# Optimization experiments

Measured on AMD Instinct MI355X. Metric: run time of the kernel, lower is better.

## Reference

```python
import jax, jax.numpy as jnp
import numpy as np
import math

NUM_HEADS = 8
DROPOUT_RATE = 0.1
D_IN = 32
D_PROJ = 32 * 16  # 512
B, SQ, SK = 8, 2048, 2048


def setup_inputs() -> dict:
    key = jax.random.key(0)
    ks = jax.random.split(key, 10)
    inv = 1.0 / math.sqrt(D_IN)
    return {
        "query": jax.random.normal(ks[0], (B, SQ, D_IN), dtype=jnp.float32),
        "key": jax.random.normal(ks[1], (B, SK, D_IN), dtype=jnp.float32),
        "value": jax.random.normal(ks[2], (B, SK, D_IN), dtype=jnp.float32),
        "mask": jax.random.randint(ks[3], (B, 1, 1, SK), 0, 2, dtype=jnp.int32),
        "Wq": jax.random.normal(ks[4], (D_PROJ, D_IN), dtype=jnp.float32) * inv,
        "bq": jax.random.normal(ks[5], (D_PROJ,), dtype=jnp.float32) * 0.02,
        "Wk": jax.random.normal(ks[6], (D_PROJ, D_IN), dtype=jnp.float32) * inv,
        "bk": jax.random.normal(ks[7], (D_PROJ,), dtype=jnp.float32) * 0.02,
        "Wv": jax.random.normal(ks[8], (D_PROJ, D_IN), dtype=jnp.float32) * inv,
        "bv": jax.random.normal(ks[9], (D_PROJ,), dtype=jnp.float32) * 0.02,
    }


def _split_heads(x):
    # [B, S, H*D] -> [B, H, S, D]
    b, s, _ = x.shape
    return x.reshape(b, s, NUM_HEADS, D_PROJ // NUM_HEADS).transpose(0, 2, 1, 3)


def reference(query, key, value, mask, Wq, bq, Wk, bk, Wv, bv):
    q = _split_heads(query @ Wq.T + bq)   # [B, H, Sq, D]
    k = _split_heads(key @ Wk.T + bk)     # [B, H, Sk, D]
    v = _split_heads(value @ Wv.T + bv)   # [B, H, Sk, D]

    head_dim = q.shape[-1]
    # mask only feeds this scalar; max(1-p, (1-p)/(Sm2*Sm3)) == 1-p for Sm2*Sm3 >= 1
    keep = 1.0 - DROPOUT_RATE
    scale_factor = jnp.maximum(jnp.float32(keep),
                               jnp.float32(keep / (mask.shape[2] * mask.shape[3])))

    scores = jnp.einsum("bhqd,bhkd->bhqk", q, k) * (scale_factor / math.sqrt(head_dim))
    probs = jax.nn.softmax(scores, axis=-1)
    # dropout treated as identity (eval mode) for a deterministic reference
    out = jnp.einsum("bhqk,bhkd->bhqd", probs, v)  # [B, H, Sq, D]
    b, h, sq, d = out.shape
    return out.transpose(0, 2, 1, 3).reshape(b, sq, h * d)
```

## Files before the change

### kernel.cpp

```cpp
#include <hip/hip_runtime.h>
#include <hip/hip_bf16.h>
#include <math.h>

#define B_   8
#define H_   8
#define S_   2048
#define D_   64
#define BH_  64
#define DPROJ_ 512

typedef __attribute__((ext_vector_type(8)))  _Float16 f16x8;
typedef __attribute__((ext_vector_type(4)))  float    f32x4;
typedef __attribute__((ext_vector_type(16))) float    f32x16;
typedef __attribute__((ext_vector_type(4)))  int      i32x4;

static __device__ __forceinline__ short f16bits(float f) {
    return __builtin_bit_cast(short, (_Float16)f);
}

static __device__ __forceinline__ f16x8 load8_f32_f16(const float* p) {
    const float4 a = ((const float4*)p)[0];
    const float4 b = ((const float4*)p)[1];
    f16x8 r;
    r[0] = (_Float16)a.x; r[1] = (_Float16)a.y; r[2] = (_Float16)a.z; r[3] = (_Float16)a.w;
    r[4] = (_Float16)b.x; r[5] = (_Float16)b.y; r[6] = (_Float16)b.z; r[7] = (_Float16)b.w;
    return r;
}

#if __has_builtin(__builtin_amdgcn_exp2f)
#define EXP2(x) __builtin_amdgcn_exp2f(x)
#else
#define EXP2(x) exp2f(x)
#endif

static __device__ __forceinline__ void pl32swap(unsigned int& a, unsigned int& b) {
#if __has_builtin(__builtin_amdgcn_permlane32_swap)
    auto r = __builtin_amdgcn_permlane32_swap((int)a, (int)b, false, false);
    a = (unsigned int)r[0];
    b = (unsigned int)r[1];
#else
    const bool lh0 = ((threadIdx.x & 63) < 32);
    unsigned int xa = (unsigned int)__shfl_xor((int)a, 32);
    unsigned int xb = (unsigned int)__shfl_xor((int)b, 32);
    unsigned int na = lh0 ? a : xb;
    unsigned int nb = lh0 ? xa : b;
    a = na; b = nb;
#endif
}

#define QKST 520

__global__ __launch_bounds__(256)
void proj_kernel(const float* __restrict__ query, const float* __restrict__ key,
                 const float* __restrict__ value,
                 const float* __restrict__ Wq, const float* __restrict__ bq,
                 const float* __restrict__ Wk, const float* __restrict__ bk,
                 const float* __restrict__ Wv, const float* __restrict__ bv,
                 short* __restrict__ qws, short* __restrict__ kws,
                 short* __restrict__ vws)
{
    __shared__ __align__(16) short shbuf[16384];

    const int tid  = threadIdx.x;
    const int wave = tid >> 6;
    const int lane = tid & 63;
    const int n    = lane & 15;
    const int quad = lane >> 4;
    const int kind = blockIdx.y;

    if (kind < 2) {
        short* tile = shbuf;
        const int r0   = blockIdx.x * 16;
        const int b    = r0 >> 11;
        const int s0   = r0 & 2047;
        const float QS = 0.16230319188537014f;

        const float* X    = kind ? key : query;
        const float* W    = kind ? Wk  : Wq;
        const float* bias = kind ? bk  : bq;
        short*       ows  = kind ? kws : qws;

        f16x8 af = load8_f32_f16(X + (r0 + n) * 32 + quad * 8);
        #pragma unroll
        for (int i = 0; i < 8; ++i) {
            const int c0 = wave * 128 + i * 16;
            f16x8 bfr = load8_f32_f16(W + (c0 + n) * 32 + quad * 8);
            f32x4 acc = {0.f, 0.f, 0.f, 0.f};
            acc = __builtin_amdgcn_mfma_f32_16x16x32_f16(af, bfr, acc, 0, 0, 0);
            const int c = c0 + n;
            const float bsf = bias[c];
            #pragma unroll
            for (int r = 0; r < 4; ++r) {
                float v = acc[r] + bsf;
                if (kind == 0) v *= QS;
                tile[(quad * 4 + r) * QKST + c] = f16bits(v);
            }
        }
        __syncthreads();

        #pragma unroll
        for (int k = 0; k < 4; ++k) {
            const int slot = k * 256 + tid;
            const int li   = slot & 7;
            const int chunk= slot >> 3;
            const int row  = chunk & 15;
            const int h    = chunk >> 4;
            uint4 vv = *(const uint4*)(tile + row * QKST + h * 64 + li * 8);
            *(uint4*)(ows + ((size_t)(b * 8 + h) * S_ + s0 + row) * 64 + li * 8) = vv;
        }
    } else {
        if (blockIdx.x >= 256) return;
        short* vtile = shbuf;
        const int r0   = blockIdx.x * 64;
        const int cb   = 0;
        const int b    = r0 >> 11;
        const int s0   = r0 & 2047;
        const int sub  = wave >> 1;
        const int sh   = (wave & 1) * 16;

        #pragma unroll
        for (int half = 0; half < 2; ++half) {
            const int cbh = half * 256;
            f16x8 bfr = load8_f32_f16(value + (r0 + sub * 32 + sh + n) * 32 + quad * 8);
            #pragma unroll
            for (int i = 0; i < 16; ++i) {
                const int c0 = cbh + i * 16;
                f16x8 af = load8_f32_f16(Wv + (c0 + n) * 32 + quad * 8);
                f32x4 acc = {0.f, 0.f, 0.f, 0.f};
                acc = __builtin_amdgcn_mfma_f32_16x16x32_f16(af, bfr, acc, 0, 0, 0);
                #pragma unroll
                for (int r = 0; r < 4; ++r) {
                    const int dc = c0 + quad * 4 + r;
                    float v = acc[r] + bv[dc];
                    vtile[(sub * 256 + (dc - cbh)) * 32 + sh + n] = f16bits(v);
                }
            }
            __syncthreads();

            #pragma unroll
            for (int k = 0; k < 8; ++k) {
                const int slot = k * 256 + tid;
                const int li   = slot & 3;
                const int cl   = (slot >> 2) & 255;
                const int sb   = slot >> 10;
                const int c    = cbh + cl;
                const int bh   = b * 8 + (c >> 6);
                const int d    = c & 63;
                const int stile= (s0 >> 5) + sb;
                uint4 vv = *(const uint4*)(vtile + (sb * 256 + cl) * 32 + li * 8);
                *(uint4*)(vws + (((size_t)bh * (S_ / 32) + stile) * 64 + d) * 32 + li * 8) = vv;
            }
            if (half == 0) __syncthreads();
        }
        (void)cb;
    }
}

#define KST 72
#define VST 40
#define OTS 36

__global__ __launch_bounds__(256, 3)
void flash_kernel(const short* __restrict__ qws, const short* __restrict__ kws,
                  const short* __restrict__ vws, float* __restrict__ out)
{
    __shared__ __align__(16) short ldsk[2 * 32 * KST];
    __shared__ __align__(16) short ldsv[2 * 64 * VST];
    __shared__ __align__(16) float olds[4 * 32 * OTS];

    const int tid  = threadIdx.x;
    const int wave = tid >> 6;
    const int lane = tid & 63;
    const int m32  = lane & 31;
    const int lh   = lane >> 5;
    const int koff = lh * 8;
    const int bh   = blockIdx.x;
    const int q0   = blockIdx.y * 256 + wave * 64;

    const short* qbase = qws + (size_t)bh * S_ * D_;
    const short* kbase = kws + (size_t)bh * S_ * D_;
    const short* vbase = vws + (size_t)bh * (S_ / 32) * 2048;

    short* kdst0 = ldsk + (tid >> 3) * KST + (tid & 7) * 8;
    short* vdst0 = ldsv + (tid >> 2) * VST + (tid & 3) * 8;

    f16x8 qb[2][4];
    #pragma unroll
    for (int qg = 0; qg < 2; ++qg)
        #pragma unroll
        for (int h = 0; h < 4; ++h)
            qb[qg][h] = *(const f16x8*)(qbase + (q0 + qg * 32 + m32) * D_ + h * 16 + koff);

    f32x16 z16;
    #pragma unroll
    for (int r = 0; r < 16; ++r) z16[r] = 0.f;

    f32x16 o[2][2];
    float  pl[2] = {0.f, 0.f};
    #pragma unroll
    for (int qg = 0; qg < 2; ++qg)
        #pragma unroll
        for (int t = 0; t < 2; ++t)
            o[qg][t] = z16;

    {
        uint4 kr = *(const uint4*)(kbase + (size_t)tid * 8);
        uint4 vr = *(const uint4*)(vbase + (size_t)tid * 8);
        *(uint4*)kdst0 = kr;
        *(uint4*)vdst0 = vr;
    }
    __syncthreads();

    for (int it = 0; it < 64; ++it) {
        const int cur = it & 1, nx = cur ^ 1;

        uint4 kr, vr;
        if (it < 63) {
            kr = *(const uint4*)(kbase + (size_t)(it + 1) * 2048 + tid * 8);
            vr = *(const uint4*)(vbase + (size_t)(it + 1) * 2048 + tid * 8);
        }

        const short* kl = ldsk + cur * (32 * KST);
        const short* vl = ldsv + cur * (64 * VST);
        f16x8 kf[4], va[4];
        #pragma unroll
        for (int h = 0; h < 4; ++h)
            kf[h] = *(const f16x8*)(kl + m32 * KST + h * 16 + koff);
        #pragma unroll
        for (int t = 0; t < 2; ++t)
            #pragma unroll
            for (int kh = 0; kh < 2; ++kh)
                va[t * 2 + kh] = *(const f16x8*)(vl + (t * 32 + m32) * VST + kh * 16 + koff);

        #pragma unroll
        for (int qg = 0; qg < 2; ++qg) {
            f32x16 st = __builtin_amdgcn_mfma_f32_32x32x16_f16(kf[0], qb[qg][0], z16, 0, 0, 0);
            #pragma unroll
            for (int h = 1; h < 4; ++h)
                st = __builtin_amdgcn_mfma_f32_32x32x16_f16(kf[h], qb[qg][h], st, 0, 0, 0);

            float p[16];
            #pragma unroll
            for (int r = 0; r < 16; ++r) p[r] = EXP2(st[r]);
            float s01 = (p[0]+p[1]) + (p[2]+p[3]);
            float s23 = (p[4]+p[5]) + (p[6]+p[7]);
            float s45 = (p[8]+p[9]) + (p[10]+p[11]);
            float s67 = (p[12]+p[13]) + (p[14]+p[15]);
            pl[qg] += (s01 + s23) + (s45 + s67);

            unsigned int pk[8];
            #pragma unroll
            for (int i = 0; i < 8; ++i)
                pk[i] = __builtin_bit_cast(unsigned int,
                          __builtin_amdgcn_cvt_pkrtz(p[2 * i], p[2 * i + 1]));
            pl32swap(pk[0], pk[2]);
            pl32swap(pk[1], pk[3]);
            pl32swap(pk[4], pk[6]);
            pl32swap(pk[5], pk[7]);

            i32x4 bi0, bi1;
            bi0[0] = (int)pk[0]; bi0[1] = (int)pk[1];
            bi0[2] = (int)pk[2]; bi0[3] = (int)pk[3];
            bi1[0] = (int)pk[4]; bi1[1] = (int)pk[5];
            bi1[2] = (int)pk[6]; bi1[3] = (int)pk[7];
            f16x8 bf0 = __builtin_bit_cast(f16x8, bi0);
            f16x8 bf1 = __builtin_bit_cast(f16x8, bi1);

            #pragma unroll
            for (int t = 0; t < 2; ++t) {
                o[qg][t] = __builtin_amdgcn_mfma_f32_32x32x16_f16(va[t * 2 + 0], bf0, o[qg][t], 0, 0, 0);
                o[qg][t] = __builtin_amdgcn_mfma_f32_32x32x16_f16(va[t * 2 + 1], bf1, o[qg][t], 0, 0, 0);
            }
        }

        __syncthreads();
        if (it < 63) {
            *(uint4*)(kdst0 + nx * (32 * KST)) = kr;
            *(uint4*)(vdst0 + nx * (64 * VST)) = vr;
        }
        __syncthreads();
    }

    const int b = bh >> 3, h = bh & 7;
    float* ow = olds + wave * (32 * OTS);
    #pragma unroll
    for (int qg = 0; qg < 2; ++qg) {
        float rs = pl[qg] + __shfl_xor(pl[qg], 32);
        float rl = 1.0f / rs;
        #pragma unroll
        for (int t = 0; t < 2; ++t) {
            const f32x16& ot = o[qg][t];
            #pragma unroll
            for (int g = 0; g < 4; ++g) {
                f32x4 w;
                w[0] = ot[g * 4 + 0] * rl;
                w[1] = ot[g * 4 + 1] * rl;
                w[2] = ot[g * 4 + 2] * rl;
                w[3] = ot[g * 4 + 3] * rl;
                *(f32x4*)(ow + m32 * OTS + 8 * g + 4 * lh) = w;
            }
            #pragma unroll
            for (int c = 0; c < 4; ++c) {
                const int row = (lane >> 3) + 8 * c;
                f32x4 v = *(const f32x4*)(ow + row * OTS + (lane & 7) * 4);
                const int sq = q0 + qg * 32 + row;
                *(f32x4*)(out + ((size_t)(b * S_ + sq)) * DPROJ_
                              + h * 64 + t * 32 + (lane & 7) * 4) = v;
            }
        }
    }
}

extern "C" void kernel_launch(void* const* d_in, const int* in_sizes, int n_in,
                              void* d_out, int out_size, void* d_ws, size_t ws_size,
                              hipStream_t stream)
{
    const float* query = (const float*)d_in[0];
    const float* key   = (const float*)d_in[1];
    const float* value = (const float*)d_in[2];
    const float* Wq = (const float*)d_in[4];
    const float* bq = (const float*)d_in[5];
    const float* Wk = (const float*)d_in[6];
    const float* bk = (const float*)d_in[7];
    const float* Wv = (const float*)d_in[8];
    const float* bv = (const float*)d_in[9];

    float* out = (float*)d_out;
    short* ws  = (short*)d_ws;
    const size_t TSZ = (size_t)BH_ * S_ * D_;
    short* qws = ws;
    short* kws = ws + TSZ;
    short* vws = ws + 2 * TSZ;

    proj_kernel<<<dim3((B_ * S_) / 16, 3), 256, 0, stream>>>(
        query, key, value, Wq, bq, Wk, bk, Wv, bv, qws, kws, vws);
    flash_kernel<<<dim3(BH_, S_ / 256), 256, 0, stream>>>(qws, kws, vws, out);
}
```

Measured before the change: 184.9 us.

## Shrink flash blocks to two waves, alias LDS output buffer, add MFMA priority hints

The flash kernel now runs 128-thread blocks covering 128 queries each, so the grid doubles and each thread loads two K/V chunks per tile instead of one. The K/V double buffers and the output staging area share one LDS pool, which cuts shared memory per block. s_setprio raises wave priority around the MFMA sequences to help interleave matrix work with softmax across waves. The trade-off is that each K/V tile is loaded from global memory by twice as many blocks, and there are more per-block barriers.

Result: slower. 280.8 us (+51.9%).

```diff
diff --git a/kernel.cpp b/kernel.cpp
--- a/kernel.cpp
+++ b/kernel.cpp
@@ -112,7 +112,6 @@
         if (blockIdx.x >= 256) return;
         short* vtile = shbuf;
         const int r0   = blockIdx.x * 64;
-        const int cb   = 0;
         const int b    = r0 >> 11;
         const int s0   = r0 & 2047;
         const int sub  = wave >> 1;
@@ -152,7 +151,6 @@
             }
             if (half == 0) __syncthreads();
         }
-        (void)cb;
     }
 }
 
@@ -160,13 +158,16 @@
 #define VST 40
 #define OTS 36
 
-__global__ __launch_bounds__(256, 3)
+#define KBUF_SH (2 * 32 * KST)
+#define VBUF_SH (2 * 64 * VST)
+
+__global__ __launch_bounds__(128, 3)
 void flash_kernel(const short* __restrict__ qws, const short* __restrict__ kws,
                   const short* __restrict__ vws, float* __restrict__ out)
 {
-    __shared__ __align__(16) short ldsk[2 * 32 * KST];
-    __shared__ __align__(16) short ldsv[2 * 64 * VST];
-    __shared__ __align__(16) float olds[4 * 32 * OTS];
+    __shared__ __align__(16) char pool[19456];
+    short* ldsk = (short*)pool;
+    short* ldsv = (short*)pool + KBUF_SH;
 
     const int tid  = threadIdx.x;
     const int wave = tid >> 6;
@@ -175,14 +176,16 @@
     const int lh   = lane >> 5;
     const int koff = lh * 8;
     const int bh   = blockIdx.x;
-    const int q0   = blockIdx.y * 256 + wave * 64;
+    const int q0   = blockIdx.y * 128 + wave * 64;
 
     const short* qbase = qws + (size_t)bh * S_ * D_;
     const short* kbase = kws + (size_t)bh * S_ * D_;
     const short* vbase = vws + (size_t)bh * (S_ / 32) * 2048;
 
     short* kdst0 = ldsk + (tid >> 3) * KST + (tid & 7) * 8;
+    short* kdst1 = kdst0 + 16 * KST;
     short* vdst0 = ldsv + (tid >> 2) * VST + (tid & 3) * 8;
+    short* vdst1 = vdst0 + 32 * VST;
 
     f16x8 qb[2][4];
     #pragma unroll
@@ -204,20 +207,25 @@
             o[qg][t] = z16;
 
     {
-        uint4 kr = *(const uint4*)(kbase + (size_t)tid * 8);
-        uint4 vr = *(const uint4*)(vbase + (size_t)tid * 8);
-        *(uint4*)kdst0 = kr;
-        *(uint4*)vdst0 = vr;
+        uint4 k0 = *(const uint4*)(kbase + (size_t)tid * 8);
+        uint4 k1 = *(const uint4*)(kbase + (size_t)tid * 8 + 1024);
+        uint4 v0 = *(const uint4*)(vbase + (size_t)tid * 8);
+        uint4 v1 = *(const uint4*)(vbase + (size_t)tid * 8 + 1024);
+        *(uint4*)kdst0 = k0;  *(uint4*)kdst1 = k1;
+        *(uint4*)vdst0 = v0;  *(uint4*)vdst1 = v1;
     }
     __syncthreads();
 
     for (int it = 0; it < 64; ++it) {
         const int cur = it & 1, nx = cur ^ 1;
 
-        uint4 kr, vr;
+        uint4 k0, k1, v0, v1;
         if (it < 63) {
-            kr = *(const uint4*)(kbase + (size_t)(it + 1) * 2048 + tid * 8);
-            vr = *(const uint4*)(vbase + (size_t)(it + 1) * 2048 + tid * 8);
+            const size_t tb = (size_t)(it + 1) * 2048 + tid * 8;
+            k0 = *(const uint4*)(kbase + tb);
+            k1 = *(const uint4*)(kbase + tb + 1024);
+            v0 = *(const uint4*)(vbase + tb);
+            v1 = *(const uint4*)(vbase + tb + 1024);
         }
 
         const short* kl = ldsk + cur * (32 * KST);
@@ -234,10 +242,12 @@
 
         #pragma unroll
         for (int qg = 0; qg < 2; ++qg) {
+            __builtin_amdgcn_s_setprio(1);
             f32x16 st = __builtin_amdgcn_mfma_f32_32x32x16_f16(kf[0], qb[qg][0], z16, 0, 0, 0);
             #pragma unroll
             for (int h = 1; h < 4; ++h)
                 st = __builtin_amdgcn_mfma_f32_32x32x16_f16(kf[h], qb[qg][h], st, 0, 0, 0);
+            __builtin_amdgcn_s_setprio(0);
 
             float p[16];
             #pragma unroll
@@ -266,23 +276,27 @@
             f16x8 bf0 = __builtin_bit_cast(f16x8, bi0);
             f16x8 bf1 = __builtin_bit_cast(f16x8, bi1);
 
+            __builtin_amdgcn_s_setprio(1);
             #pragma unroll
             for (int t = 0; t < 2; ++t) {
                 o[qg][t] = __builtin_amdgcn_mfma_f32_32x32x16_f16(va[t * 2 + 0], bf0, o[qg][t], 0, 0, 0);
                 o[qg][t] = __builtin_amdgcn_mfma_f32_32x32x16_f16(va[t * 2 + 1], bf1, o[qg][t], 0, 0, 0);
             }
+            __builtin_amdgcn_s_setprio(0);
         }
 
         __syncthreads();
         if (it < 63) {
-            *(uint4*)(kdst0 + nx * (32 * KST)) = kr;
-            *(uint4*)(vdst0 + nx * (64 * VST)) = vr;
+            *(uint4*)(kdst0 + nx * (32 * KST)) = k0;
+            *(uint4*)(kdst1 + nx * (32 * KST)) = k1;
+            *(uint4*)(vdst0 + nx * (64 * VST)) = v0;
+            *(uint4*)(vdst1 + nx * (64 * VST)) = v1;
         }
         __syncthreads();
     }
 
     const int b = bh >> 3, h = bh & 7;
-    float* ow = olds + wave * (32 * OTS);
+    float* ow = (float*)pool + wave * (32 * OTS);
     #pragma unroll
     for (int qg = 0; qg < 2; ++qg) {
         float rs = pl[qg] + __shfl_xor(pl[qg], 32);
@@ -334,5 +348,5 @@
 
     proj_kernel<<<dim3((B_ * S_) / 16, 3), 256, 0, stream>>>(
         query, key, value, Wq, bq, Wk, bk, Wv, bv, qws, kws, vws);
-    flash_kernel<<<dim3(BH_, S_ / 256), 256, 0, stream>>>(qws, kws, vws, out);
-}
+    flash_kernel<<<dim3(BH_, S_ / 128), 128, 0, stream>>>(qws, kws, vws, out);
+}
```
